# Kernel tuning notes

Hardware: AMD Instinct MI355X
Metric: run time of the kernel (lower is better)

## Reference

```python
import jax, jax.numpy as jnp
import numpy as np

T, B, D = 1024, 256, 256


def setup_inputs() -> dict:
    key = jax.random.key(0)
    ks = jax.random.split(key, 8)
    s = 1.0 / np.sqrt(D).astype(np.float32)
    x = jax.random.normal(ks[0], (T, B, D), jnp.float32)
    # episode-reset flags; sparse like real RL rollouts
    resets = jax.random.bernoulli(ks[1], 0.01, (T, B))
    # flax GRUCell params: input kernels (with bias) for gates [r|z|n],
    # hidden kernels (no bias except 'hn' which has one)
    Wi = jax.random.normal(ks[2], (D, 3 * D), jnp.float32) * s  # [ir|iz|in]
    bi = jnp.zeros((3 * D,), jnp.float32)
    Whr = jax.random.normal(ks[3], (D, D), jnp.float32) * s
    Whz = jax.random.normal(ks[4], (D, D), jnp.float32) * s
    Whn = jax.random.normal(ks[5], (D, D), jnp.float32) * s
    bhn = jnp.zeros((D,), jnp.float32)
    return {"x": x, "resets": resets, "Wi": Wi, "bi": bi,
            "Whr": Whr, "Whz": Whz, "Whn": Whn, "bhn": bhn}


def reference(x, resets, Wi, bi, Whr, Whz, Whn, bhn):
    # Precompute all input projections in one big GEMM: (T,B,3D)
    xp = jnp.einsum('tbd,dh->tbh', x, Wi) + bi
    xr, xz, xn = jnp.split(xp, 3, axis=-1)
    h0 = jnp.zeros((x.shape[1], Whr.shape[0]), x.dtype)

    def step(h, inp):
        xr_t, xz_t, xn_t, reset_t = inp
        # reset masking: reinitialize carry to zeros where episode ended
        h = jnp.where(reset_t[:, None], jnp.zeros_like(h), h)
        # flax.linen.GRUCell math
        r = jax.nn.sigmoid(xr_t + h @ Whr)
        z = jax.nn.sigmoid(xz_t + h @ Whz)
        n = jnp.tanh(xn_t + r * (h @ Whn + bhn))
        h_new = (1.0 - z) * n + z * h
        return h_new, h_new  # GRUCell returns (new_carry, y=new_carry)

    _, ys = jax.lax.scan(step, h0, (xr, xz, xn, resets))
    return ys  # (T, B, D)
```

## Files before the change

### kernel.cpp

```cpp
#include <hip/hip_runtime.h>


typedef __attribute__((ext_vector_type(8))) short short8;
typedef __attribute__((ext_vector_type(4))) float f32x4;

#define T_DIM 1024
#define B_DIM 256
#define D_DIM 256
#define SCL_RZ (-1.44269504f)
#define SCL_N  (2.88539008f)

__device__ __forceinline__ unsigned short f2bf(float f) {
  union { float f; unsigned u; } c; c.f = f;
  unsigned r = c.u + 0x7FFFu + ((c.u >> 16) & 1u);
  return (unsigned short)(r >> 16);
}
__device__ __forceinline__ float u2f(unsigned u) {
  union { unsigned u; float f; } c; c.u = u;
  return c.f;
}
__device__ __forceinline__ float dpp_shr4(float own, float src) {
  union { float f; int i; } o, s, r;
  o.f = own; s.f = src;
  r.i = __builtin_amdgcn_update_dpp(o.i, s.i, 0x114, 0xF, 0xA, false);
  return r.f;
}
__device__ __forceinline__ float dpp_shr8(float own, float src) {
  union { float f; int i; } o, s, r;
  o.f = own; s.f = src;
  r.i = __builtin_amdgcn_update_dpp(o.i, s.i, 0x118, 0xF, 0xC, false);
  return r.f;
}
__device__ __forceinline__ float dpp_shr2(float x) {
  union { float f; int i; } s, r;
  s.f = x;
  r.i = __builtin_amdgcn_update_dpp(s.i, s.i, 0x112, 0xF, 0xF, false);
  return r.f;
}

__global__ void detect_resets(const int* __restrict__ r, int n, int* __restrict__ flags) {
  int isf = 0, oth = 0;
  for (int i = blockIdx.x * blockDim.x + threadIdx.x; i < n; i += gridDim.x * blockDim.x) {
    int v = r[i];
    if (v == 0x3F800000) isf = 1;
    else if (v != 0 && v != 1) oth = 1;
  }
  if (isf) atomicOr(&flags[0], 1);
  if (oth) atomicOr(&flags[1], 1);
}

__device__ __forceinline__ int read_reset(const void* r, int f0, int f1, int idx) {
  if (f0) return ((const float*)r)[idx] != 0.0f;
  if (f1) return ((const unsigned char*)r)[idx] != 0;
  return ((const int*)r)[idx] != 0;
}

__global__ void convert_resets(const void* __restrict__ rst, const int* __restrict__ flags,
                               unsigned char* __restrict__ rst8) {
  int f0 = flags[0], f1 = flags[1];
  for (int i = blockIdx.x * blockDim.x + threadIdx.x; i < T_DIM * B_DIM;
       i += gridDim.x * blockDim.x)
    rst8[i] = (unsigned char)read_reset(rst, f0, f1, i);
}

__global__ void pack_weights(const float* __restrict__ Wi,
                             const float* __restrict__ Whr,
                             const float* __restrict__ Whz,
                             const float* __restrict__ Whn,
                             unsigned short* __restrict__ WiT,
                             unsigned short* __restrict__ Wpk) {
  int gid = blockIdx.x * 256 + threadIdx.x;
  const int NE = 768 * 256;
  if (gid < NE) {
    int n = gid >> 8, k = gid & 255;
    float scl = (n < 512) ? SCL_RZ : SCL_N;
    WiT[gid] = f2bf(Wi[k * 768 + n] * scl);
  } else if (gid < 2 * NE) {
    int g = gid - NE;
    int j = g & 7, l = (g >> 3) & 63, ks = (g >> 9) & 7, nt = g >> 12;
    int k = ks * 32 + (l >> 4) * 8 + j;
    int col = nt * 16 + (l & 15);
    float w;
    if (col < 256)      w = Whr[k * 256 + col] * SCL_RZ;
    else if (col < 512) w = Whz[k * 256 + col - 256] * SCL_RZ;
    else                w = Whn[k * 256 + col - 512] * SCL_N;
    Wpk[g] = f2bf(w);
  }
}

__global__ __launch_bounds__(256) void gemm_xp(
    const float* __restrict__ x, const unsigned short* __restrict__ WiT,
    const float* __restrict__ bi, unsigned short* __restrict__ xp) {
  __shared__ __align__(16) unsigned short Al[128 * 64];
  __shared__ __align__(16) unsigned short Bl[128 * 64];
  const int tid = threadIdx.x;
  const int l = tid & 63, wid = tid >> 6;
  const int wm = wid >> 1, wn = wid & 1;
  const int L = blockIdx.x, nwg = gridDim.x;
  const int q = nwg >> 3, r8 = nwg & 7;
  const int c = L & 7, o = L >> 3;
  const int g = c * q + ((c < r8) ? c : r8) + o;
  const int n0 = (g % 6) * 128;
  const long m0 = (long)(g / 6) * 128;
  f32x4 acc[4][4] = {};
  for (int kb = 0; kb < 4; ++kb) {
    const int k0 = kb * 64;
    if (kb) __syncthreads();
#pragma unroll
    for (int i = 0; i < 8; ++i) {
      int fidx = i * 256 + tid;
      int row = fidx >> 4, kf = fidx & 15;
      float4 v = *(const float4*)&x[(m0 + row) * 256 + k0 + kf * 4];
      uint2 p;
      p.x = f2bf(v.x) | ((unsigned)f2bf(v.y) << 16);
      p.y = f2bf(v.z) | ((unsigned)f2bf(v.w) << 16);
      int byte = (row * 128 + kf * 8) ^ ((row & 7) << 4);
      *(uint2*)((char*)Al + byte) = p;
    }
#pragma unroll
    for (int i = 0; i < 4; ++i) {
      int cidx = i * 256 + tid;
      int row = cidx >> 3, kc = cidx & 7;
      short8 v = *(const short8*)&WiT[(n0 + row) * 256 + k0 + kc * 8];
      int byte = (row * 128 + kc * 16) ^ ((row & 7) << 4);
      *(short8*)((char*)Bl + byte) = v;
    }
    __syncthreads();
#pragma unroll
    for (int kk = 0; kk < 2; ++kk) {
      short8 af[4], bfv[4];
#pragma unroll
      for (int t = 0; t < 4; ++t) {
        int m = wm * 64 + t * 16 + (l & 15);
        af[t] = *(const short8*)((char*)Al + ((m * 128 + kk * 64 + (l >> 4) * 16) ^ ((m & 7) << 4)));
        int n = wn * 64 + t * 16 + (l & 15);
        bfv[t] = *(const short8*)((char*)Bl + ((n * 128 + kk * 64 + (l >> 4) * 16) ^ ((n & 7) << 4)));
      }
#pragma unroll
      for (int tm = 0; tm < 4; ++tm)
#pragma unroll
        for (int tn = 0; tn < 4; ++tn)
          acc[tm][tn] = __builtin_amdgcn_mfma_f32_16x16x32_bf16(af[tm], bfv[tn], acc[tm][tn], 0, 0, 0);
    }
  }
#pragma unroll
  for (int tn = 0; tn < 4; ++tn) {
    int n = n0 + wn * 64 + tn * 16 + (l & 15);
    float bscl = bi[n] * ((n < 512) ? SCL_RZ : SCL_N);
#pragma unroll
    for (int tm = 0; tm < 4; ++tm) {
#pragma unroll
      for (int r = 0; r < 4; ++r) {
        long m = m0 + wm * 64 + tm * 16 + (l >> 4) * 4 + r;
        xp[m * 768 + n] = f2bf(acc[tm][tn][r] + bscl);
      }
    }
  }
}

__global__ __launch_bounds__(512, 2) void rnn_scan(
    const unsigned short* __restrict__ xp, const unsigned char* __restrict__ rst8,
    const float* __restrict__ bhn, const unsigned short* __restrict__ Wpk,
    float* __restrict__ y, float* __restrict__ hws, int t0, int Tc) {
  __shared__ __align__(16) unsigned short hb16[2][2 * 256];
  const int tid = threadIdx.x;
  const int l = tid & 63, w = tid >> 6;
  const int p = l & 15, grp = l >> 4;
  const int b = p & 1;
  const int B0 = blockIdx.x * 2;
  const bool odd1 = (p >> 1) & 1;
  const int d0 = w * 32 + ((p >> 2) & 1) * 16 + grp * 4 + ((p >> 3) & 1) * 2 + ((p >> 1) & 1);

  short8 wreg[48];
#pragma unroll
  for (int t = 0; t < 6; ++t) {
    int dt = (t >> 1) * 16 + w * 2 + (t & 1);
#pragma unroll
    for (int kk = 0; kk < 8; ++kk)
      wreg[t * 8 + kk] = *(const short8*)&Wpk[((dt * 8 + kk) * 64 + l) * 8];
  }
  const float bh = bhn[d0] * SCL_N;

  float h = 0.f;
  if (t0 > 0) {
    float hv = hws[(B0 + b) * 256 + d0];
    if (!rst8[t0 * 256 + B0 + b]) h = hv;
  }
  {
    unsigned hp;
    asm("v_cvt_pk_bf16_f32 %0, %1, %2" : "=v"(hp) : "v"(h), "v"(h));
    *(unsigned short*)((char*)&hb16[0][0] + b * 512 + d0 * 2) = (unsigned short)hp;
  }
  __syncthreads();

  const unsigned short* xpp = xp + ((long)(B0 + b)) * 768 + d0;
  float* yp = y + ((long)t0 * 256 + B0 + b) * 256 + d0;
  unsigned xr_ = *(const unsigned short*)(xpp);
  unsigned xz_ = *(const unsigned short*)(xpp + 256);
  unsigned xn_ = *(const unsigned short*)(xpp + 512);
  xpp += 256 * 768;
  int rstn = (t0 + 1 < T_DIM) ? (int)rst8[(t0 + 1) * 256 + B0 + b] : 0;
  const char* hrd = (const char*)&hb16[0][0] + b * 512 + grp * 16;
  char* hwr = (char*)&hb16[0][0] + b * 512 + d0 * 2;

  for (int ts = 0; ts < Tc; ++ts) {
    const int cur = ts & 1, nxt = cur ^ 1;
    const char* hb = hrd + cur * 1024;
    short8 hfr[3];
#define LD_H(k) (*(const short8*)(hb + (k) * 64))
    hfr[0] = LD_H(0);
    hfr[1] = LD_H(1);
    f32x4 acc[6] = {};
    __builtin_amdgcn_s_setprio(1);
#pragma unroll
    for (int kk = 0; kk < 8; ++kk) {
      if (kk + 2 < 8) hfr[(kk + 2) % 3] = LD_H(kk + 2);
      const int s = kk % 3;
      acc[0] = __builtin_amdgcn_mfma_f32_16x16x32_bf16(wreg[kk],      hfr[s], acc[0], 0, 0, 0);
      acc[1] = __builtin_amdgcn_mfma_f32_16x16x32_bf16(wreg[8 + kk],  hfr[s], acc[1], 0, 0, 0);
      acc[2] = __builtin_amdgcn_mfma_f32_16x16x32_bf16(wreg[16 + kk], hfr[s], acc[2], 0, 0, 0);
      acc[3] = __builtin_amdgcn_mfma_f32_16x16x32_bf16(wreg[24 + kk], hfr[s], acc[3], 0, 0, 0);
      acc[4] = __builtin_amdgcn_mfma_f32_16x16x32_bf16(wreg[32 + kk], hfr[s], acc[4], 0, 0, 0);
      acc[5] = __builtin_amdgcn_mfma_f32_16x16x32_bf16(wreg[40 + kk], hfr[s], acc[5], 0, 0, 0);
    }
    __builtin_amdgcn_s_setprio(0);
#undef LD_H
    float aR, aZ, aN;
    {
      float f0, f1, f2, f3, g0, g1;
      f0 = dpp_shr4(acc[0][0], acc[1][0]); f1 = dpp_shr4(acc[0][1], acc[1][1]);
      f2 = dpp_shr4(acc[0][2], acc[1][2]); f3 = dpp_shr4(acc[0][3], acc[1][3]);
      g0 = dpp_shr8(f0, f2); g1 = dpp_shr8(f1, f3);
      aR = odd1 ? dpp_shr2(g1) : g0;
      f0 = dpp_shr4(acc[2][0], acc[3][0]); f1 = dpp_shr4(acc[2][1], acc[3][1]);
      f2 = dpp_shr4(acc[2][2], acc[3][2]); f3 = dpp_shr4(acc[2][3], acc[3][3]);
      g0 = dpp_shr8(f0, f2); g1 = dpp_shr8(f1, f3);
      aZ = odd1 ? dpp_shr2(g1) : g0;
      f0 = dpp_shr4(acc[4][0], acc[5][0]); f1 = dpp_shr4(acc[4][1], acc[5][1]);
      f2 = dpp_shr4(acc[4][2], acc[5][2]); f3 = dpp_shr4(acc[4][3], acc[5][3]);
      g0 = dpp_shr8(f0, f2); g1 = dpp_shr8(f1, f3);
      aN = odd1 ? dpp_shr2(g1) : g0;
    }
    float den_r = 1.0f + exp2f(fminf(u2f(xr_ << 16) + aR, 14.f));
    float den_z = 1.0f + exp2f(fminf(u2f(xz_ << 16) + aZ, 14.f));
    float s = __builtin_amdgcn_rcpf(den_r * den_z);
    float rg = den_z * s;
    float zg = den_r * s;
    float cden = 1.0f + exp2f(fminf(fmaf(rg, aN + bh, u2f(xn_ << 16)), 14.f));
    float ic = __builtin_amdgcn_rcpf(cden);
    float ng = fmaf(-2.0f, ic, 1.0f);
    float o = fmaf(zg, h - ng, ng);
    *yp = o;
    yp += 256 * 256;
    h = rstn ? 0.f : o;
    {
      unsigned hp;
      asm("v_cvt_pk_bf16_f32 %0, %1, %2" : "=v"(hp) : "v"(h), "v"(h));
      *(unsigned short*)(hwr + nxt * 1024) = (unsigned short)hp;
    }
    if (ts + 1 < Tc) {
      xr_ = *(const unsigned short*)(xpp);
      xz_ = *(const unsigned short*)(xpp + 256);
      xn_ = *(const unsigned short*)(xpp + 512);
      xpp += 256 * 768;
      int tg = t0 + ts;
      rstn = (tg + 2 < T_DIM) ? (int)rst8[(tg + 2) * 256 + B0 + b] : 0;
    }
    asm volatile("s_waitcnt lgkmcnt(0)" ::: "memory");
    __builtin_amdgcn_s_barrier();
  }
  hws[(B0 + b) * 256 + d0] = h;
}

extern "C" void kernel_launch(void* const* d_in, const int* in_sizes, int n_in,
                              void* d_out, int out_size, void* d_ws, size_t ws_size,
                              hipStream_t stream) {
  const float* x    = (const float*)d_in[0];
  const void*  rst  = d_in[1];
  const float* Wi   = (const float*)d_in[2];
  const float* bi   = (const float*)d_in[3];
  const float* Whr  = (const float*)d_in[4];
  const float* Whz  = (const float*)d_in[5];
  const float* Whn  = (const float*)d_in[6];
  const float* bhn  = (const float*)d_in[7];
  float* y = (float*)d_out;

  char* ws = (char*)d_ws;
  unsigned short* Wpk = (unsigned short*)(ws);
  unsigned short* WiT = (unsigned short*)(ws + 393216);
  float* hws          = (float*)(ws + 786432);
  int* flags          = (int*)(ws + 1048576);
  unsigned char* rst8 = (unsigned char*)(ws + 1048832);
  unsigned short* xpb = (unsigned short*)(ws + 1310976);

  const size_t fixed = 1310976;
  int Tc = T_DIM;
  while (Tc > 1 && fixed + (size_t)Tc * B_DIM * 768 * 2 > ws_size) Tc >>= 1;

  hipMemsetAsync(flags, 0, 8, stream);
  detect_resets<<<64, 256, 0, stream>>>((const int*)rst, T_DIM * B_DIM / 4, flags);
  convert_resets<<<256, 256, 0, stream>>>(rst, flags, rst8);
  pack_weights<<<1536, 256, 0, stream>>>(Wi, Whr, Whz, Whn, WiT, Wpk);
  for (int t0 = 0; t0 < T_DIM; t0 += Tc) {
    gemm_xp<<<12 * Tc, 256, 0, stream>>>(x + (long)t0 * B_DIM * D_DIM, WiT, bi, xpb);
    rnn_scan<<<128, 512, 0, stream>>>(xpb, rst8, bhn, Wpk, y, hws, t0, Tc);
  }
}
```

Measured before the change: 1.486 ms.

## Fuse input-projection GEMM and GRU scan into one producer/consumer kernel

Merges the input-projection GEMM and the recurrent scan into a single launch of 256 blocks. Odd blocks compute xp in rounds of 128 row-tiles and publish completion through per-round atomic counters, while even blocks run the scan and spin-wait on those counters before reading each timestep's projections. This overlaps the large GEMM with the latency-bound serial scan instead of running them back to back. It also packs two bf16 hidden values per LDS store via a DPP swap. The design relies on producer and consumer blocks being co-resident, and the spin-waits risk stalls or deadlock if they are not.

```diff
diff --git a/kernel.cpp b/kernel.cpp
--- a/kernel.cpp
+++ b/kernel.cpp
@@ -35,6 +35,12 @@
   union { float f; int i; } s, r;
   s.f = x;
   r.i = __builtin_amdgcn_update_dpp(s.i, s.i, 0x112, 0xF, 0xF, false);
+  return r.f;
+}
+__device__ __forceinline__ float dpp_swap2(float x) {
+  union { float f; int i; } s, r;
+  s.f = x;
+  r.i = __builtin_amdgcn_update_dpp(s.i, s.i, 0x4E, 0xF, 0xF, false);
   return r.f;
 }
 
@@ -88,86 +94,100 @@
   }
 }
 
-__global__ __launch_bounds__(256) void gemm_xp(
+__global__ __launch_bounds__(512, 2) void fused(
     const float* __restrict__ x, const unsigned short* __restrict__ WiT,
-    const float* __restrict__ bi, unsigned short* __restrict__ xp) {
-  __shared__ __align__(16) unsigned short Al[128 * 64];
-  __shared__ __align__(16) unsigned short Bl[128 * 64];
+    const float* __restrict__ bi, unsigned short* __restrict__ xp,
+    const unsigned char* __restrict__ rst8, const float* __restrict__ bhn,
+    const unsigned short* __restrict__ Wpk, float* __restrict__ y,
+    float* __restrict__ hws, int* __restrict__ rc, int t0, int Tc) {
+  __shared__ __align__(16) char smem[32768];
   const int tid = threadIdx.x;
-  const int l = tid & 63, wid = tid >> 6;
-  const int wm = wid >> 1, wn = wid & 1;
-  const int L = blockIdx.x, nwg = gridDim.x;
-  const int q = nwg >> 3, r8 = nwg & 7;
-  const int c = L & 7, o = L >> 3;
-  const int g = c * q + ((c < r8) ? c : r8) + o;
-  const int n0 = (g % 6) * 128;
-  const long m0 = (long)(g / 6) * 128;
-  f32x4 acc[4][4] = {};
-  for (int kb = 0; kb < 4; ++kb) {
-    const int k0 = kb * 64;
-    if (kb) __syncthreads();
-#pragma unroll
-    for (int i = 0; i < 8; ++i) {
-      int fidx = i * 256 + tid;
-      int row = fidx >> 4, kf = fidx & 15;
-      float4 v = *(const float4*)&x[(m0 + row) * 256 + k0 + kf * 4];
-      uint2 p;
-      p.x = f2bf(v.x) | ((unsigned)f2bf(v.y) << 16);
-      p.y = f2bf(v.z) | ((unsigned)f2bf(v.w) << 16);
-      int byte = (row * 128 + kf * 8) ^ ((row & 7) << 4);
-      *(uint2*)((char*)Al + byte) = p;
-    }
-#pragma unroll
-    for (int i = 0; i < 4; ++i) {
-      int cidx = i * 256 + tid;
-      int row = cidx >> 3, kc = cidx & 7;
-      short8 v = *(const short8*)&WiT[(n0 + row) * 256 + k0 + kc * 8];
-      int byte = (row * 128 + kc * 16) ^ ((row & 7) << 4);
-      *(short8*)((char*)Bl + byte) = v;
-    }
-    __syncthreads();
-#pragma unroll
-    for (int kk = 0; kk < 2; ++kk) {
-      short8 af[4], bfv[4];
-#pragma unroll
-      for (int t = 0; t < 4; ++t) {
-        int m = wm * 64 + t * 16 + (l & 15);
-        af[t] = *(const short8*)((char*)Al + ((m * 128 + kk * 64 + (l >> 4) * 16) ^ ((m & 7) << 4)));
-        int n = wn * 64 + t * 16 + (l & 15);
-        bfv[t] = *(const short8*)((char*)Bl + ((n * 128 + kk * 64 + (l >> 4) * 16) ^ ((n & 7) << 4)));
+
+  if (blockIdx.x & 1) {
+    unsigned short* Al = (unsigned short*)smem;
+    unsigned short* Bl = (unsigned short*)(smem + 16384);
+    const int pw = blockIdx.x >> 1;
+    const int l = tid & 63, wid = tid >> 6;
+    const int wm = wid >> 2, wn = wid & 3;
+    const int Mc = Tc * 2;
+    const int rounds = (Mc + 127) >> 7;
+    for (int r = 0; r < rounds; ++r) {
+      const int mb = r * 128 + pw;
+      if (mb < Mc) {
+        const long m0 = (long)mb * 128;
+        for (int nb = 0; nb < 6; ++nb) {
+          const int n0 = nb * 128;
+          f32x4 acc[4][2] = {};
+          for (int kb = 0; kb < 4; ++kb) {
+            const int k0 = kb * 64;
+            __syncthreads();
+#pragma unroll
+            for (int i = 0; i < 4; ++i) {
+              int fidx = i * 512 + tid;
+              int row = fidx >> 4, kf = fidx & 15;
+              float4 v = *(const float4*)&x[(m0 + row) * 256 + k0 + kf * 4];
+              uint2 pk;
+              pk.x = f2bf(v.x) | ((unsigned)f2bf(v.y) << 16);
+              pk.y = f2bf(v.z) | ((unsigned)f2bf(v.w) << 16);
+              int byte = (row * 128 + kf * 8) ^ ((row & 7) << 4);
+              *(uint2*)((char*)Al + byte) = pk;
+            }
+#pragma unroll
+            for (int i = 0; i < 2; ++i) {
+              int cidx = i * 512 + tid;
+              int row = cidx >> 3, kc = cidx & 7;
+              short8 v = *(const short8*)&WiT[(n0 + row) * 256 + k0 + kc * 8];
+              int byte = (row * 128 + kc * 16) ^ ((row & 7) << 4);
+              *(short8*)((char*)Bl + byte) = v;
+            }
+            __syncthreads();
+#pragma unroll
+            for (int kk = 0; kk < 2; ++kk) {
+              short8 af[4], bfv[2];
+#pragma unroll
+              for (int t = 0; t < 4; ++t) {
+                int m = wm * 64 + t * 16 + (l & 15);
+                af[t] = *(const short8*)((char*)Al + ((m * 128 + kk * 64 + (l >> 4) * 16) ^ ((m & 7) << 4)));
+              }
+#pragma unroll
+              for (int u = 0; u < 2; ++u) {
+                int n = wn * 32 + u * 16 + (l & 15);
+                bfv[u] = *(const short8*)((char*)Bl + ((n * 128 + kk * 64 + (l >> 4) * 16) ^ ((n & 7) << 4)));
+              }
+#pragma unroll
+              for (int tm = 0; tm < 4; ++tm)
+#pragma unroll
+                for (int tn = 0; tn < 2; ++tn)
+                  acc[tm][tn] = __builtin_amdgcn_mfma_f32_16x16x32_bf16(af[tm], bfv[tn], acc[tm][tn], 0, 0, 0);
+            }
+          }
+#pragma unroll
+          for (int tn = 0; tn < 2; ++tn) {
+            int n = n0 + wn * 32 + tn * 16 + (l & 15);
+            float bscl = bi[n] * ((n < 512) ? SCL_RZ : SCL_N);
+#pragma unroll
+            for (int tm = 0; tm < 4; ++tm) {
+#pragma unroll
+              for (int rr = 0; rr < 4; ++rr) {
+                long m = m0 + wm * 64 + tm * 16 + (l >> 4) * 4 + rr;
+                xp[m * 768 + n] = f2bf(acc[tm][tn][rr] + bscl);
+              }
+            }
+          }
+        }
       }
-#pragma unroll
-      for (int tm = 0; tm < 4; ++tm)
-#pragma unroll
-        for (int tn = 0; tn < 4; ++tn)
-          acc[tm][tn] = __builtin_amdgcn_mfma_f32_16x16x32_bf16(af[tm], bfv[tn], acc[tm][tn], 0, 0, 0);
-    }
-  }
-#pragma unroll
-  for (int tn = 0; tn < 4; ++tn) {
-    int n = n0 + wn * 64 + tn * 16 + (l & 15);
-    float bscl = bi[n] * ((n < 512) ? SCL_RZ : SCL_N);
-#pragma unroll
-    for (int tm = 0; tm < 4; ++tm) {
-#pragma unroll
-      for (int r = 0; r < 4; ++r) {
-        long m = m0 + wm * 64 + tm * 16 + (l >> 4) * 4 + r;
-        xp[m * 768 + n] = f2bf(acc[tm][tn][r] + bscl);
-      }
-    }
-  }
-}
-
-__global__ __launch_bounds__(512, 2) void rnn_scan(
-    const unsigned short* __restrict__ xp, const unsigned char* __restrict__ rst8,
-    const float* __restrict__ bhn, const unsigned short* __restrict__ Wpk,
-    float* __restrict__ y, float* __restrict__ hws, int t0, int Tc) {
-  __shared__ __align__(16) unsigned short hb16[2][2 * 256];
-  const int tid = threadIdx.x;
+      __syncthreads();
+      if (tid == 0)
+        __hip_atomic_fetch_add(&rc[r], 1, __ATOMIC_RELEASE, __HIP_MEMORY_SCOPE_AGENT);
+    }
+    return;
+  }
+
+  unsigned short* hb16 = (unsigned short*)smem;
   const int l = tid & 63, w = tid >> 6;
   const int p = l & 15, grp = l >> 4;
   const int b = p & 1;
-  const int B0 = blockIdx.x * 2;
+  const int B0 = (blockIdx.x >> 1) * 2;
   const bool odd1 = (p >> 1) & 1;
   const int d0 = w * 32 + ((p >> 2) & 1) * 16 + grp * 4 + ((p >> 3) & 1) * 2 + ((p >> 1) & 1);
 
@@ -189,9 +209,19 @@
   {
     unsigned hp;
     asm("v_cvt_pk_bf16_f32 %0, %1, %2" : "=v"(hp) : "v"(h), "v"(h));
-    *(unsigned short*)((char*)&hb16[0][0] + b * 512 + d0 * 2) = (unsigned short)hp;
+    *(unsigned short*)((char*)hb16 + b * 512 + d0 * 2) = (unsigned short)hp;
   }
   __syncthreads();
+
+  int done_rounds = 0;
+#define WAIT_ROUNDS(rneed)                                                              \
+  while (done_rounds <= (rneed)) {                                                     \
+    int c_ = __hip_atomic_load(&rc[done_rounds], __ATOMIC_ACQUIRE,                     \
+                               __HIP_MEMORY_SCOPE_AGENT);                              \
+    if (c_ == 128) ++done_rounds;                                                      \
+    else __builtin_amdgcn_s_sleep(8);                                                  \
+  }
+  WAIT_ROUNDS(0)
 
   const unsigned short* xpp = xp + ((long)(B0 + b)) * 768 + d0;
   float* yp = y + ((long)t0 * 256 + B0 + b) * 256 + d0;
@@ -200,8 +230,8 @@
   unsigned xn_ = *(const unsigned short*)(xpp + 512);
   xpp += 256 * 768;
   int rstn = (t0 + 1 < T_DIM) ? (int)rst8[(t0 + 1) * 256 + B0 + b] : 0;
-  const char* hrd = (const char*)&hb16[0][0] + b * 512 + grp * 16;
-  char* hwr = (char*)&hb16[0][0] + b * 512 + d0 * 2;
+  const char* hrd = (const char*)hb16 + b * 512 + grp * 16;
+  char* hwr = (char*)hb16 + b * 512 + d0 * 2;
 
   for (int ts = 0; ts < Tc; ++ts) {
     const int cur = ts & 1, nxt = cur ^ 1;
@@ -254,11 +284,15 @@
     yp += 256 * 256;
     h = rstn ? 0.f : o;
     {
-      unsigned hp;
-      asm("v_cvt_pk_bf16_f32 %0, %1, %2" : "=v"(hp) : "v"(h), "v"(h));
-      *(unsigned short*)(hwr + nxt * 1024) = (unsigned short)hp;
+      float hq = dpp_swap2(h);
+      if ((p & 2) == 0) {
+        unsigned hp;
+        asm("v_cvt_pk_bf16_f32 %0, %1, %2" : "=v"(hp) : "v"(h), "v"(hq));
+        *(unsigned*)(hwr + nxt * 1024) = hp;
+      }
     }
     if (ts + 1 < Tc) {
+      WAIT_ROUNDS((2 * ts + 3) >> 7)
       xr_ = *(const unsigned short*)(xpp);
       xz_ = *(const unsigned short*)(xpp + 256);
       xn_ = *(const unsigned short*)(xpp + 512);
@@ -269,6 +303,7 @@
     asm volatile("s_waitcnt lgkmcnt(0)" ::: "memory");
     __builtin_amdgcn_s_barrier();
   }
+#undef WAIT_ROUNDS
   hws[(B0 + b) * 256 + d0] = h;
 }
 
@@ -290,6 +325,7 @@
   unsigned short* WiT = (unsigned short*)(ws + 393216);
   float* hws          = (float*)(ws + 786432);
   int* flags          = (int*)(ws + 1048576);
+  int* rc             = (int*)(ws + 1048640);
   unsigned char* rst8 = (unsigned char*)(ws + 1048832);
   unsigned short* xpb = (unsigned short*)(ws + 1310976);
 
@@ -302,7 +338,8 @@
   convert_resets<<<256, 256, 0, stream>>>(rst, flags, rst8);
   pack_weights<<<1536, 256, 0, stream>>>(Wi, Whr, Whz, Whn, WiT, Wpk);
   for (int t0 = 0; t0 < T_DIM; t0 += Tc) {
-    gemm_xp<<<12 * Tc, 256, 0, stream>>>(x + (long)t0 * B_DIM * D_DIM, WiT, bi, xpb);
-    rnn_scan<<<128, 512, 0, stream>>>(xpb, rst8, bhn, Wpk, y, hws, t0, Tc);
-  }
-}
+    hipMemsetAsync(rc, 0, 64, stream);
+    fused<<<256, 512, 0, stream>>>(x + (long)t0 * B_DIM * D_DIM, WiT, bi, xpb,
+                                   rst8, bhn, Wpk, y, hws, rc, t0, Tc);
+  }
+}
```

Result: faster. 1.224 ms (median of 2 runs) (-17.7%).
